# Kernel tuning notes

Hardware: AMD Instinct MI355X
Metric: run time of the kernel (lower is better)

## Reference

```python
import jax, jax.numpy as jnp
import numpy as np

N, E, D, DE, DH = 8000, 15000, 128, 16, 128
NUM_STEPS = 3


def setup_inputs() -> dict:
    key = jax.random.key(0)
    ks = jax.random.split(key, 10)
    s = lambda k, shape, scale: jax.random.normal(k, shape, jnp.float32) * scale
    return {
        "x": jax.random.normal(ks[0], (N, D), jnp.float32),
        "edge_attr": jax.random.normal(ks[1], (E, DE), jnp.float32),
        "W0": s(ks[2], (D, D), 0.08),   # lin0
        "b0": jnp.zeros((D,), jnp.float32),
        "W1": s(ks[3], (DE, DH), 0.2),  # edge net layer 1
        "b1": jnp.zeros((DH,), jnp.float32),
        "W2": s(ks[4], (DH, D * D), 0.02),  # edge net layer 2 -> D*D
        "b2": jnp.zeros((D * D,), jnp.float32),
        "root": s(ks[5], (D, D), 0.08),  # NNConv root weight
        "bias": jnp.zeros((D,), jnp.float32),  # NNConv bias
        "Wm": s(ks[6], (2 * D, D), 0.08),  # message_layer
        "bm": jnp.zeros((D,), jnp.float32),
        "edge_index": jax.random.randint(ks[7], (2, E), 0, N, jnp.int32),
    }


def reference(x, edge_attr, W0, b0, W1, b1, W2, b2, root, bias, Wm, bm, edge_index):
    n, d = x.shape
    src, dst = edge_index[0], edge_index[1]  # source_to_target flow (PyG default)
    # edge-conditioned weight matrices, identical across steps since edge_attr is fixed: [E, D, D]
    ew = (jax.nn.relu(edge_attr @ W1 + b1) @ W2 + b2).reshape(-1, d, d)
    init = x
    out = jax.nn.relu(x @ W0 + b0)
    for _ in range(NUM_STEPS):
        # gather source features, per-edge matvec, scatter-add to destinations
        msg = jnp.einsum('ed,edo->eo', out[src], ew)  # [E, D]
        agg = jax.ops.segment_sum(msg, dst, num_segments=n)  # [N, D]
        m = jax.nn.relu(agg + out @ root + bias)  # NNConv with root_weight + bias, then relu
        out = jnp.concatenate([m, out], axis=1) @ Wm + bm  # message_layer
    return out + init
```

## Files before the change

kernel.cpp:

```cpp
#include <hip/hip_runtime.h>

#define NE   15000
#define NVX  8000
#define EPAD 15104
#define NT_E 118

typedef __attribute__((ext_vector_type(8))) short short8;
typedef __attribute__((ext_vector_type(4))) float f32x4;

static __device__ __forceinline__ unsigned short f2b(float f){
  unsigned int u = __float_as_uint(f);
  u += 0x7fffu + ((u >> 16) & 1u);
  return (unsigned short)(u >> 16);
}

__global__ __launch_bounds__(256) void k_cvt(const float* __restrict__ in,
                                             unsigned short* __restrict__ out, int n){
  int i = (blockIdx.x * 256 + threadIdx.x) * 4;
  if (i >= n) return;
  float4 v = *(const float4*)(in + i);
  ushort4 o;
  o.x = f2b(v.x); o.y = f2b(v.y); o.z = f2b(v.z); o.w = f2b(v.w);
  *(ushort4*)(out + i) = o;
}

__global__ __launch_bounds__(256) void k_h1(const float* __restrict__ ea,
                                            const float* __restrict__ W1,
                                            const float* __restrict__ b1,
                                            float* __restrict__ h1T){
  __shared__ float sW1[16*128];
  __shared__ float sb1[128];
  int t = threadIdx.x;
  #pragma unroll
  for (int i = 0; i < 8; ++i) sW1[i*256 + t] = W1[i*256 + t];
  if (t < 128) sb1[t] = b1[t];
  __syncthreads();
  int e = blockIdx.x * 64 + (t & 63);
  int hg = t >> 6;
  bool valid = e < NE;
  int esafe = valid ? e : 0;
  float a[16];
  #pragma unroll
  for (int i = 0; i < 4; ++i){
    float4 v = *(const float4*)(ea + (size_t)esafe*16 + i*4);
    a[i*4+0]=v.x; a[i*4+1]=v.y; a[i*4+2]=v.z; a[i*4+3]=v.w;
  }
  for (int hh = 0; hh < 32; ++hh){
    int h = hg*32 + hh;
    float s = sb1[h];
    #pragma unroll
    for (int k = 0; k < 16; ++k) s = fmaf(a[k], sW1[k*128 + h], s);
    s = fmaxf(s, 0.f);
    h1T[(size_t)h*EPAD + e] = valid ? s : 0.f;
  }
}

__global__ __launch_bounds__(256) void k_wt(const float* __restrict__ W2,
                                            const float* __restrict__ b2,
                                            const float* __restrict__ W0,
                                            const float* __restrict__ root,
                                            const float* __restrict__ Wm,
                                            unsigned short* __restrict__ W2T,
                                            unsigned short* __restrict__ sWt){
  int b = blockIdx.x;
  const float* src;
  unsigned short* out;
  if (b < 128)      { src = W2 + (size_t)b*16384; out = W2T + (size_t)b*16384; }
  else if (b == 128){ src = b2;                   out = W2T + (size_t)128*16384; }
  else {
    int s = b - 129;
    out = sWt + (size_t)s*16384;
    src = (s==0) ? W0 : (s==1) ? root : (s==2) ? Wm : (Wm + 128*128);
  }
  int t = threadIdx.x;
  int o = t & 127, half = t >> 7;
  for (int it = 0; it < 8; ++it){
    int d0 = half*64 + it*8;
    unsigned int pk[4];
    #pragma unroll
    for (int j = 0; j < 4; ++j){
      float v0 = src[(size_t)(d0 + 2*j    )*128 + o];
      float v1 = src[(size_t)(d0 + 2*j + 1)*128 + o];
      pk[j] = (unsigned int)f2b(v0) | ((unsigned int)f2b(v1) << 16);
    }
    unsigned int off = (unsigned int)(o*256 + d0*2) ^ (((unsigned int)(o & 7)) << 4);
    *(uint4*)((char*)out + off) = make_uint4(pk[0], pk[1], pk[2], pk[3]);
  }
}

__global__ __launch_bounds__(512,2) void k_big(const unsigned short* __restrict__ outcur,
                                               const unsigned short* __restrict__ W2T,
                                               const float* __restrict__ h1T,
                                               const int* __restrict__ eidx,
                                               float* __restrict__ agg){
  __shared__ __align__(16) unsigned short sX[128*128];
  int t = threadIdx.x, l = t & 63, w = t >> 6;
  int tile = blockIdx.x >> 1, par = blockIdx.x & 1;
  int e0 = tile * 128;
  {
    int r = t >> 2, q = t & 3;
    int e = e0 + r;
    int srow = eidx[e < NE ? e : NE-1];
    const uint4* gp = (const uint4*)(outcur + (size_t)srow*128);
    #pragma unroll
    for (int i = 0; i < 4; ++i){
      uint4 v = gp[q*4 + i];
      unsigned off = (unsigned)((q*64 + i*16) ^ ((r & 7) << 4));
      *(uint4*)((char*)sX + r*256 + off) = v;
    }
  }
  __syncthreads();
  short8 af[8][4];
  #pragma unroll
  for (int mf = 0; mf < 8; ++mf){
    int row = mf*16 + (l & 15);
    #pragma unroll
    for (int kf = 0; kf < 4; ++kf){
      unsigned off = (unsigned)((kf*64 + ((l >> 4)*16)) ^ ((row & 7) << 4));
      af[mf][kf] = *(const short8*)((const char*)sX + row*256 + off);
    }
  }
  f32x4 acc[8];
  #pragma unroll
  for (int mf = 0; mf < 8; ++mf) acc[mf] = (f32x4){0.f,0.f,0.f,0.f};
  int colc = w*16 + (l & 15);
  unsigned offB[4];
  #pragma unroll
  for (int kf = 0; kf < 4; ++kf)
    offB[kf] = (unsigned)((colc*256 + kf*64 + ((l >> 4)*16)) ^ ((colc & 7) << 4));
  const float* hbase = h1T + e0 + ((l >> 4) << 2);
  const char* wb2 = (const char*)W2T;
  const f32x4 zf = (f32x4){0.f,0.f,0.f,0.f};
  int nh = 64 + ((par == 0) ? 1 : 0);
  for (int hh = 0; hh < nh; ++hh){
    int h = (hh < 64) ? (par + 2*hh) : 128;
    const char* wb = wb2 + (size_t)h * 32768;
    short8 bq[4];
    #pragma unroll
    for (int kf = 0; kf < 4; ++kf) bq[kf] = *(const short8*)(wb + offB[kf]);
    const float* hp = hbase + (size_t)h * EPAD;
    #pragma unroll
    for (int half = 0; half < 2; ++half){
      f32x4 Y[4];
      #pragma unroll
      for (int kf = 0; kf < 4; ++kf)
        #pragma unroll
        for (int m4 = 0; m4 < 4; ++m4)
          Y[m4] = __builtin_amdgcn_mfma_f32_16x16x32_bf16(af[half*4+m4][kf], bq[kf],
                    (kf == 0) ? zf : Y[m4], 0, 0, 0);
      f32x4 hv[4];
      if (hh < 64){
        #pragma unroll
        for (int m4 = 0; m4 < 4; ++m4) hv[m4] = *(const f32x4*)(hp + (half*4+m4)*16);
      } else {
        #pragma unroll
        for (int m4 = 0; m4 < 4; ++m4){
          int rb = e0 + (half*4+m4)*16 + ((l >> 4) << 2);
          #pragma unroll
          for (int j = 0; j < 4; ++j) hv[m4][j] = (rb + j < NE) ? 1.f : 0.f;
        }
      }
      #pragma unroll
      for (int m4 = 0; m4 < 4; ++m4)
        #pragma unroll
        for (int j = 0; j < 4; ++j)
          acc[half*4+m4][j] = fmaf(hv[m4][j], Y[m4][j], acc[half*4+m4][j]);
    }
  }
  #pragma unroll
  for (int mf = 0; mf < 8; ++mf){
    #pragma unroll
    for (int j = 0; j < 4; ++j){
      int e = e0 + mf*16 + ((l >> 4) << 2) + j;
      int dst = (e < NE) ? eidx[NE + e] : 0;
      atomicAdd(agg + (size_t)dst*128 + colc, acc[mf][j]);
    }
  }
}

__global__ __launch_bounds__(256,2) void k_gsm(const unsigned short* __restrict__ Aa,
                                               const unsigned short* __restrict__ Wa,
                                               const unsigned short* __restrict__ Ab,
                                               const unsigned short* __restrict__ Wb,
                                               const float* __restrict__ addin,
                                               float* __restrict__ clr,
                                               const float* __restrict__ bias,
                                               int do_relu,
                                               unsigned short* __restrict__ outb,
                                               float* __restrict__ outf){
  __shared__ __align__(16) unsigned short sA[64*128];
  __shared__ __align__(16) unsigned short sW[128*128];
  int t = threadIdx.x, l = t & 63, w = t >> 6;
  int r0 = blockIdx.x * 64;
  f32x4 acc[4][2];
  #pragma unroll
  for (int mf = 0; mf < 4; ++mf)
    #pragma unroll
    for (int nf = 0; nf < 2; ++nf)
      acc[mf][nf] = (f32x4){0.f,0.f,0.f,0.f};
  const unsigned short* A = Aa;
  const unsigned short* W = Wa;
  for (int pass = 0; pass < 2; ++pass){
    if (pass == 1){
      if (Ab == nullptr) break;
      A = Ab; W = Wb;
      __syncthreads();
    }
    {
      const uint4* gp = (const uint4*)((const char*)A + (size_t)r0*256);
      uint4* lp = (uint4*)sA;
      #pragma unroll
      for (int i = 0; i < 4; ++i) lp[i*256 + t] = gp[i*256 + t];
      const uint4* gw = (const uint4*)W;
      uint4* lw = (uint4*)sW;
      #pragma unroll
      for (int i = 0; i < 8; ++i) lw[i*256 + t] = gw[i*256 + t];
    }
    __syncthreads();
    short8 af[4][4];
    #pragma unroll
    for (int mf = 0; mf < 4; ++mf)
      #pragma unroll
      for (int kf = 0; kf < 4; ++kf)
        af[mf][kf] = *(const short8*)((const char*)sA + (mf*16 + (l & 15))*256 + kf*64 + ((l >> 4)*16));
    #pragma unroll
    for (int nf = 0; nf < 2; ++nf){
      int col = w*32 + nf*16 + (l & 15);
      unsigned int swz = ((unsigned int)(col & 7)) << 4;
      #pragma unroll
      for (int kf = 0; kf < 4; ++kf){
        short8 bfr = *(const short8*)((const char*)sW +
                        (((unsigned int)(col*256 + kf*64 + ((l >> 4)*16))) ^ swz));
        #pragma unroll
        for (int mf = 0; mf < 4; ++mf)
          acc[mf][nf] = __builtin_amdgcn_mfma_f32_16x16x32_bf16(af[mf][kf], bfr, acc[mf][nf], 0, 0, 0);
      }
    }
  }
  #pragma unroll
  for (int mf = 0; mf < 4; ++mf){
    #pragma unroll
    for (int nf = 0; nf < 2; ++nf){
      #pragma unroll
      for (int j = 0; j < 4; ++j){
        int r = r0 + mf*16 + ((l >> 4) << 2) + j;
        int c = w*32 + nf*16 + (l & 15);
        float v = acc[mf][nf][j];
        if (addin) v += addin[(size_t)r*128 + c];
        if (clr)   clr[(size_t)r*128 + c] = 0.f;
        v += bias[c];
        if (do_relu) v = fmaxf(v, 0.f);
        if (outb) outb[(size_t)r*128 + c] = f2b(v);
        if (outf) outf[(size_t)r*128 + c] = v;
      }
    }
  }
}

extern "C" void kernel_launch(void* const* d_in, const int* in_sizes, int n_in,
                              void* d_out, int out_size, void* d_ws, size_t ws_size,
                              hipStream_t stream){
  (void)in_sizes; (void)n_in; (void)out_size; (void)ws_size;
  const float* x    = (const float*)d_in[0];
  const float* ea   = (const float*)d_in[1];
  const float* W0   = (const float*)d_in[2];
  const float* b0   = (const float*)d_in[3];
  const float* W1   = (const float*)d_in[4];
  const float* b1   = (const float*)d_in[5];
  const float* W2   = (const float*)d_in[6];
  const float* b2   = (const float*)d_in[7];
  const float* root = (const float*)d_in[8];
  const float* bias = (const float*)d_in[9];
  const float* Wm   = (const float*)d_in[10];
  const float* bm   = (const float*)d_in[11];
  const int*   eidx = (const int*)d_in[12];

  char* p = (char*)d_ws;
  unsigned short* W2T = (unsigned short*)p; p += (size_t)129*32768;
  unsigned short* sWt = (unsigned short*)p; p += (size_t)4*32768;
  float*          h1T = (float*)p;          p += (size_t)128*EPAD*4;
  unsigned short* xb  = (unsigned short*)p; p += (size_t)NVX*128*2;
  unsigned short* oA  = (unsigned short*)p; p += (size_t)NVX*128*2;
  unsigned short* oB  = (unsigned short*)p; p += (size_t)NVX*128*2;
  unsigned short* mB  = (unsigned short*)p; p += (size_t)NVX*128*2;
  float*          agg = (float*)p;          p += (size_t)NVX*128*4;

  k_cvt<<<1000, 256, 0, stream>>>(x, xb, NVX*128);
  k_h1 <<<EPAD/64, 256, 0, stream>>>(ea, W1, b1, h1T);
  k_wt <<<133,  256, 0, stream>>>(W2, b2, W0, root, Wm, W2T, sWt);
  k_gsm<<<125, 256, 0, stream>>>(xb, sWt + 0*16384,
                                 (const unsigned short*)nullptr, (const unsigned short*)nullptr,
                                 (const float*)nullptr, (float*)nullptr, b0, 1, oA, (float*)nullptr);
  unsigned short* cur = oA;
  unsigned short* nxt = oB;
  for (int s = 0; s < 3; ++s){
    if (s == 0) hipMemsetAsync(agg, 0, (size_t)NVX*128*4, stream);
    k_big<<<2*NT_E, 512, 0, stream>>>(cur, W2T, h1T, eidx, agg);
    k_gsm<<<125, 256, 0, stream>>>(cur, sWt + 1*16384,
                                   (const unsigned short*)nullptr, (const unsigned short*)nullptr,
                                   agg, (s < 2) ? agg : (float*)nullptr, bias, 1, mB, (float*)nullptr);
    if (s < 2){
      k_gsm<<<125, 256, 0, stream>>>(mB, sWt + 2*16384, cur, sWt + 3*16384,
                                     (const float*)nullptr, (float*)nullptr, bm, 0, nxt, (float*)nullptr);
    } else {
      k_gsm<<<125, 256, 0, stream>>>(mB, sWt + 2*16384, cur, sWt + 3*16384,
                                     x, (float*)nullptr, bm, 0, (unsigned short*)nullptr, (float*)d_out);
    }
    unsigned short* tsw = cur; cur = nxt; nxt = tsw;
  }
}
```

Baseline: 424.2 us.

## Prefetch W2 fragments one step ahead and stage h1 tile in LDS

The edge-net kernel now software-pipelines the per-h W2 B-fragment loads, fetching the next hidden unit's fragments while the current MFMAs run. The block's slice of h1T (64 rows x 128 edges) is staged into shared memory once up front instead of being read from global memory inside the loop. The bias (h=128) step is peeled out of the loop for the even-parity blocks. Shared memory grows by 32 KB and launch bounds drop to one 512-thread block per CU minimum, so occupancy may fall while register pressure rises from the double-buffered fragments.

```diff
diff --git a/kernel.cpp b/kernel.cpp
--- a/kernel.cpp
+++ b/kernel.cpp
@@ -88,15 +88,26 @@
   }
 }
 
-__global__ __launch_bounds__(512,2) void k_big(const unsigned short* __restrict__ outcur,
+__global__ __launch_bounds__(512,1) void k_big(const unsigned short* __restrict__ outcur,
                                                const unsigned short* __restrict__ W2T,
                                                const float* __restrict__ h1T,
                                                const int* __restrict__ eidx,
                                                float* __restrict__ agg){
   __shared__ __align__(16) unsigned short sX[128*128];
+  __shared__ __align__(16) float          sH[64*128];
   int t = threadIdx.x, l = t & 63, w = t >> 6;
   int tile = blockIdx.x >> 1, par = blockIdx.x & 1;
   int e0 = tile * 128;
+  int colc = w*16 + (l & 15);
+  unsigned offB[4];
+  #pragma unroll
+  for (int kf = 0; kf < 4; ++kf)
+    offB[kf] = (unsigned)((colc*256 + kf*64 + ((l >> 4)*16)) ^ ((colc & 7) << 4));
+  const char* wb2 = (const char*)W2T;
+  short8 bq[4];
+  #pragma unroll
+  for (int kf = 0; kf < 4; ++kf)
+    bq[kf] = *(const short8*)(wb2 + (size_t)par*32768 + offB[kf]);
   {
     int r = t >> 2, q = t & 3;
     int e = e0 + r;
@@ -109,6 +120,14 @@
       *(uint4*)((char*)sX + r*256 + off) = v;
     }
   }
+  {
+    #pragma unroll
+    for (int i = 0; i < 4; ++i){
+      int n = i*512 + t;
+      int row = n >> 5, c4 = n & 31;
+      ((f32x4*)sH)[n] = ((const f32x4*)(h1T + (size_t)(par + 2*row)*EPAD + e0))[c4];
+    }
+  }
   __syncthreads();
   short8 af[8][4];
   #pragma unroll
@@ -123,22 +142,15 @@
   f32x4 acc[8];
   #pragma unroll
   for (int mf = 0; mf < 8; ++mf) acc[mf] = (f32x4){0.f,0.f,0.f,0.f};
-  int colc = w*16 + (l & 15);
-  unsigned offB[4];
-  #pragma unroll
-  for (int kf = 0; kf < 4; ++kf)
-    offB[kf] = (unsigned)((colc*256 + kf*64 + ((l >> 4)*16)) ^ ((colc & 7) << 4));
-  const float* hbase = h1T + e0 + ((l >> 4) << 2);
-  const char* wb2 = (const char*)W2T;
   const f32x4 zf = (f32x4){0.f,0.f,0.f,0.f};
-  int nh = 64 + ((par == 0) ? 1 : 0);
-  for (int hh = 0; hh < nh; ++hh){
-    int h = (hh < 64) ? (par + 2*hh) : 128;
-    const char* wb = wb2 + (size_t)h * 32768;
-    short8 bq[4];
-    #pragma unroll
-    for (int kf = 0; kf < 4; ++kf) bq[kf] = *(const short8*)(wb + offB[kf]);
-    const float* hp = hbase + (size_t)h * EPAD;
+  #pragma unroll 2
+  for (int hh = 0; hh < 64; ++hh){
+    int hn = par + 2*hh + 2;
+    if (hn > 128) hn = 128;
+    short8 bqn[4];
+    #pragma unroll
+    for (int kf = 0; kf < 4; ++kf)
+      bqn[kf] = *(const short8*)(wb2 + (size_t)hn*32768 + offB[kf]);
     #pragma unroll
     for (int half = 0; half < 2; ++half){
       f32x4 Y[4];
@@ -149,22 +161,35 @@
           Y[m4] = __builtin_amdgcn_mfma_f32_16x16x32_bf16(af[half*4+m4][kf], bq[kf],
                     (kf == 0) ? zf : Y[m4], 0, 0, 0);
       f32x4 hv[4];
-      if (hh < 64){
-        #pragma unroll
-        for (int m4 = 0; m4 < 4; ++m4) hv[m4] = *(const f32x4*)(hp + (half*4+m4)*16);
-      } else {
-        #pragma unroll
-        for (int m4 = 0; m4 < 4; ++m4){
-          int rb = e0 + (half*4+m4)*16 + ((l >> 4) << 2);
-          #pragma unroll
-          for (int j = 0; j < 4; ++j) hv[m4][j] = (rb + j < NE) ? 1.f : 0.f;
-        }
-      }
+      #pragma unroll
+      for (int m4 = 0; m4 < 4; ++m4)
+        hv[m4] = *(const f32x4*)((const char*)sH + hh*512 + (half*4+m4)*64 + ((l >> 4)*16));
       #pragma unroll
       for (int m4 = 0; m4 < 4; ++m4)
         #pragma unroll
         for (int j = 0; j < 4; ++j)
           acc[half*4+m4][j] = fmaf(hv[m4][j], Y[m4][j], acc[half*4+m4][j]);
+    }
+    #pragma unroll
+    for (int kf = 0; kf < 4; ++kf) bq[kf] = bqn[kf];
+  }
+  if (par == 0){
+    #pragma unroll
+    for (int half = 0; half < 2; ++half){
+      f32x4 Y[4];
+      #pragma unroll
+      for (int kf = 0; kf < 4; ++kf)
+        #pragma unroll
+        for (int m4 = 0; m4 < 4; ++m4)
+          Y[m4] = __builtin_amdgcn_mfma_f32_16x16x32_bf16(af[half*4+m4][kf], bq[kf],
+                    (kf == 0) ? zf : Y[m4], 0, 0, 0);
+      #pragma unroll
+      for (int m4 = 0; m4 < 4; ++m4){
+        int rb = e0 + (half*4+m4)*16 + ((l >> 4) << 2);
+        #pragma unroll
+        for (int j = 0; j < 4; ++j)
+          if (rb + j < NE) acc[half*4+m4][j] += Y[m4][j];
+      }
     }
   }
   #pragma unroll
```

Result: faster. 359.9 us (-15.1%).

## Restructure edge-conditioned matvec kernel with smaller tiles and fragment-linear W2 layout

Applied to the files above, without the earlier changes.

The main edge kernel now uses 64-edge tiles split across output halves and h-parity, giving 940 blocks of 256 threads instead of 236 blocks of 512. W2T is stored in an MFMA-fragment-linear layout so each wave reads its weight fragments contiguously, and the next h slice is double-buffered in registers. The MFMA operands are swapped so edges sit on the N dimension. h1 values and destination indices are staged in shared memory, and s_setprio raises wave priority around the MFMA blocks. The aim is more occupancy, better latency hiding and less scattered global traffic, at the cost of more blocks re-gathering source rows and reloading W2.

```diff
diff --git a/kernel.cpp b/kernel.cpp
--- a/kernel.cpp
+++ b/kernel.cpp
@@ -3,7 +3,7 @@
 #define NE   15000
 #define NVX  8000
 #define EPAD 15104
-#define NT_E 118
+#define NT_E 235
 
 typedef __attribute__((ext_vector_type(8))) short short8;
 typedef __attribute__((ext_vector_type(4))) float f32x4;
@@ -65,6 +65,7 @@
   int b = blockIdx.x;
   const float* src;
   unsigned short* out;
+  bool fraglin = (b < 129);
   if (b < 128)      { src = W2 + (size_t)b*16384; out = W2T + (size_t)b*16384; }
   else if (b == 128){ src = b2;                   out = W2T + (size_t)128*16384; }
   else {
@@ -83,20 +84,35 @@
       float v1 = src[(size_t)(d0 + 2*j + 1)*128 + o];
       pk[j] = (unsigned int)f2b(v0) | ((unsigned int)f2b(v1) << 16);
     }
-    unsigned int off = (unsigned int)(o*256 + d0*2) ^ (((unsigned int)(o & 7)) << 4);
+    unsigned int off;
+    if (fraglin)
+      off = (unsigned)((o >> 4)*4096 + (d0 >> 5)*1024 + (((d0 >> 3) & 3)*16 + (o & 15))*16);
+    else
+      off = ((unsigned)(o*256 + d0*2)) ^ (((unsigned)(o & 7)) << 4);
     *(uint4*)((char*)out + off) = make_uint4(pk[0], pk[1], pk[2], pk[3]);
   }
 }
 
-__global__ __launch_bounds__(512,2) void k_big(const unsigned short* __restrict__ outcur,
+__global__ __launch_bounds__(256,3) void k_big(const unsigned short* __restrict__ outcur,
                                                const unsigned short* __restrict__ W2T,
                                                const float* __restrict__ h1T,
                                                const int* __restrict__ eidx,
                                                float* __restrict__ agg){
-  __shared__ __align__(16) unsigned short sX[128*128];
+  __shared__ __align__(16) unsigned short sX[64*128];
+  __shared__ __align__(16) float          sH[64*64];
+  __shared__ int sD[64];
   int t = threadIdx.x, l = t & 63, w = t >> 6;
-  int tile = blockIdx.x >> 1, par = blockIdx.x & 1;
-  int e0 = tile * 128;
+  unsigned bid = blockIdx.x;
+  int tile = bid >> 2, oh = (bid >> 1) & 1, par = bid & 1;
+  int e0 = tile * 64;
+  const char* wb2 = (const char*)W2T;
+  unsigned offA = (unsigned)((oh*4 + w)*4096 + l*16);
+  short8 aqA[4], aqB[4];
+  {
+    const char* wb = wb2 + (size_t)par*32768 + offA;
+    #pragma unroll
+    for (int kf = 0; kf < 4; ++kf) aqA[kf] = *(const short8*)(wb + kf*1024);
+  }
   {
     int r = t >> 2, q = t & 3;
     int e = e0 + r;
@@ -109,72 +125,91 @@
       *(uint4*)((char*)sX + r*256 + off) = v;
     }
   }
+  {
+    #pragma unroll
+    for (int i = 0; i < 4; ++i){
+      int n = i*256 + t;
+      int row = n >> 4, c = n & 15;
+      ((f32x4*)sH)[n] = ((const f32x4*)(h1T + (size_t)(par + 2*row)*EPAD + e0))[c];
+    }
+  }
+  if (t < 64){
+    int e = e0 + t;
+    sD[t] = (e < NE) ? eidx[NE + e] : 0;
+  }
   __syncthreads();
-  short8 af[8][4];
-  #pragma unroll
-  for (int mf = 0; mf < 8; ++mf){
-    int row = mf*16 + (l & 15);
+  short8 bfr[4][4];
+  #pragma unroll
+  for (int nf = 0; nf < 4; ++nf){
+    int row = nf*16 + (l & 15);
     #pragma unroll
     for (int kf = 0; kf < 4; ++kf){
       unsigned off = (unsigned)((kf*64 + ((l >> 4)*16)) ^ ((row & 7) << 4));
-      af[mf][kf] = *(const short8*)((const char*)sX + row*256 + off);
-    }
-  }
-  f32x4 acc[8];
-  #pragma unroll
-  for (int mf = 0; mf < 8; ++mf) acc[mf] = (f32x4){0.f,0.f,0.f,0.f};
-  int colc = w*16 + (l & 15);
-  unsigned offB[4];
-  #pragma unroll
-  for (int kf = 0; kf < 4; ++kf)
-    offB[kf] = (unsigned)((colc*256 + kf*64 + ((l >> 4)*16)) ^ ((colc & 7) << 4));
-  const float* hbase = h1T + e0 + ((l >> 4) << 2);
-  const char* wb2 = (const char*)W2T;
+      bfr[nf][kf] = *(const short8*)((const char*)sX + row*256 + off);
+    }
+  }
+  f32x4 acc[4];
+  #pragma unroll
+  for (int nf = 0; nf < 4; ++nf) acc[nf] = (f32x4){0.f,0.f,0.f,0.f};
   const f32x4 zf = (f32x4){0.f,0.f,0.f,0.f};
-  int nh = 64 + ((par == 0) ? 1 : 0);
-  for (int hh = 0; hh < nh; ++hh){
-    int h = (hh < 64) ? (par + 2*hh) : 128;
-    const char* wb = wb2 + (size_t)h * 32768;
-    short8 bq[4];
-    #pragma unroll
-    for (int kf = 0; kf < 4; ++kf) bq[kf] = *(const short8*)(wb + offB[kf]);
-    const float* hp = hbase + (size_t)h * EPAD;
-    #pragma unroll
-    for (int half = 0; half < 2; ++half){
-      f32x4 Y[4];
-      #pragma unroll
-      for (int kf = 0; kf < 4; ++kf)
+  int ecol = l & 15;
+  for (int hh = 0; hh < 64; hh += 2){
+    {
+      const char* wb = wb2 + (size_t)(par + 2*(hh+1))*32768 + offA;
+      #pragma unroll
+      for (int kf = 0; kf < 4; ++kf) aqB[kf] = *(const short8*)(wb + kf*1024);
+    }
+    __builtin_amdgcn_s_setprio(1);
+    #pragma unroll
+    for (int nf = 0; nf < 4; ++nf){
+      f32x4 Y = __builtin_amdgcn_mfma_f32_16x16x32_bf16(aqA[0], bfr[nf][0], zf, 0, 0, 0);
+      Y = __builtin_amdgcn_mfma_f32_16x16x32_bf16(aqA[1], bfr[nf][1], Y, 0, 0, 0);
+      Y = __builtin_amdgcn_mfma_f32_16x16x32_bf16(aqA[2], bfr[nf][2], Y, 0, 0, 0);
+      Y = __builtin_amdgcn_mfma_f32_16x16x32_bf16(aqA[3], bfr[nf][3], Y, 0, 0, 0);
+      float hs = sH[hh*64 + nf*16 + ecol];
+      #pragma unroll
+      for (int j = 0; j < 4; ++j) acc[nf][j] = fmaf(hs, Y[j], acc[nf][j]);
+    }
+    __builtin_amdgcn_s_setprio(0);
+    {
+      int kb = par + 2*(hh+2);
+      if (kb > 128) kb = 128;
+      const char* wb = wb2 + (size_t)kb*32768 + offA;
+      #pragma unroll
+      for (int kf = 0; kf < 4; ++kf) aqA[kf] = *(const short8*)(wb + kf*1024);
+    }
+    __builtin_amdgcn_s_setprio(1);
+    #pragma unroll
+    for (int nf = 0; nf < 4; ++nf){
+      f32x4 Y = __builtin_amdgcn_mfma_f32_16x16x32_bf16(aqB[0], bfr[nf][0], zf, 0, 0, 0);
+      Y = __builtin_amdgcn_mfma_f32_16x16x32_bf16(aqB[1], bfr[nf][1], Y, 0, 0, 0);
+      Y = __builtin_amdgcn_mfma_f32_16x16x32_bf16(aqB[2], bfr[nf][2], Y, 0, 0, 0);
+      Y = __builtin_amdgcn_mfma_f32_16x16x32_bf16(aqB[3], bfr[nf][3], Y, 0, 0, 0);
+      float hs = sH[(hh+1)*64 + nf*16 + ecol];
+      #pragma unroll
+      for (int j = 0; j < 4; ++j) acc[nf][j] = fmaf(hs, Y[j], acc[nf][j]);
+    }
+    __builtin_amdgcn_s_setprio(0);
+  }
+  if (par == 0){
+    #pragma unroll
+    for (int nf = 0; nf < 4; ++nf){
+      f32x4 Y = __builtin_amdgcn_mfma_f32_16x16x32_bf16(aqA[0], bfr[nf][0], zf, 0, 0, 0);
+      Y = __builtin_amdgcn_mfma_f32_16x16x32_bf16(aqA[1], bfr[nf][1], Y, 0, 0, 0);
+      Y = __builtin_amdgcn_mfma_f32_16x16x32_bf16(aqA[2], bfr[nf][2], Y, 0, 0, 0);
+      Y = __builtin_amdgcn_mfma_f32_16x16x32_bf16(aqA[3], bfr[nf][3], Y, 0, 0, 0);
+      if (e0 + nf*16 + ecol < NE){
         #pragma unroll
-        for (int m4 = 0; m4 < 4; ++m4)
-          Y[m4] = __builtin_amdgcn_mfma_f32_16x16x32_bf16(af[half*4+m4][kf], bq[kf],
-                    (kf == 0) ? zf : Y[m4], 0, 0, 0);
-      f32x4 hv[4];
-      if (hh < 64){
-        #pragma unroll
-        for (int m4 = 0; m4 < 4; ++m4) hv[m4] = *(const f32x4*)(hp + (half*4+m4)*16);
-      } else {
-        #pragma unroll
-        for (int m4 = 0; m4 < 4; ++m4){
-          int rb = e0 + (half*4+m4)*16 + ((l >> 4) << 2);
-          #pragma unroll
-          for (int j = 0; j < 4; ++j) hv[m4][j] = (rb + j < NE) ? 1.f : 0.f;
-        }
+        for (int j = 0; j < 4; ++j) acc[nf][j] += Y[j];
       }
-      #pragma unroll
-      for (int m4 = 0; m4 < 4; ++m4)
-        #pragma unroll
-        for (int j = 0; j < 4; ++j)
-          acc[half*4+m4][j] = fmaf(hv[m4][j], Y[m4][j], acc[half*4+m4][j]);
-    }
-  }
-  #pragma unroll
-  for (int mf = 0; mf < 8; ++mf){
-    #pragma unroll
-    for (int j = 0; j < 4; ++j){
-      int e = e0 + mf*16 + ((l >> 4) << 2) + j;
-      int dst = (e < NE) ? eidx[NE + e] : 0;
-      atomicAdd(agg + (size_t)dst*128 + colc, acc[mf][j]);
-    }
+    }
+  }
+  #pragma unroll
+  for (int nf = 0; nf < 4; ++nf){
+    int dst = sD[nf*16 + ecol];
+    float* ap = agg + (size_t)dst*128 + oh*64 + w*16 + ((l >> 4) << 2);
+    #pragma unroll
+    for (int j = 0; j < 4; ++j) atomicAdd(ap + j, acc[nf][j]);
   }
 }
 
@@ -295,7 +330,7 @@
   unsigned short* nxt = oB;
   for (int s = 0; s < 3; ++s){
     if (s == 0) hipMemsetAsync(agg, 0, (size_t)NVX*128*4, stream);
-    k_big<<<2*NT_E, 512, 0, stream>>>(cur, W2T, h1T, eidx, agg);
+    k_big<<<NT_E*4, 256, 0, stream>>>(cur, W2T, h1T, eidx, agg);
     k_gsm<<<125, 256, 0, stream>>>(cur, sWt + 1*16384,
                                    (const unsigned short*)nullptr, (const unsigned short*)nullptr,
                                    agg, (s < 2) ? agg : (float*)nullptr, bias, 1, mB, (float*)nullptr);
```

Result: slower. 456.1 us (+7.5%).

## Double-buffer W2 tiles in LDS via async loads and stage h1 in LDS

Applied to the files above, without the earlier changes.

The edge-weight GEMM kernel now streams each 32KB W2T slice into a pair of LDS buffers with global_load_lds. The load for the next h step is issued while MFMAs run on the current one. The h1 coefficients for the block's 64 h values are preloaded into LDS with nontemporal loads, and MFMA chains are interleaved with the scaling FMAs under raised wave priority. This is meant to hide global-load latency on W2 and h1 inside the inner loop. In exchange, LDS use grows to 96KB and launch bounds drop to one block per CU, which lowers occupancy.

```diff
diff --git a/kernel.cpp b/kernel.cpp
--- a/kernel.cpp
+++ b/kernel.cpp
@@ -88,15 +88,39 @@
   }
 }
 
-__global__ __launch_bounds__(512,2) void k_big(const unsigned short* __restrict__ outcur,
+__global__ __launch_bounds__(512,1) void k_big(const unsigned short* __restrict__ outcur,
                                                const unsigned short* __restrict__ W2T,
                                                const float* __restrict__ h1T,
                                                const int* __restrict__ eidx,
                                                float* __restrict__ agg){
-  __shared__ __align__(16) unsigned short sX[128*128];
+  __shared__ __align__(16) char lds[3*32768];
+  char* wbufA = lds;
+  char* wbufB = lds + 32768;
+  float* sH   = (float*)(lds + 65536);
   int t = threadIdx.x, l = t & 63, w = t >> 6;
   int tile = blockIdx.x >> 1, par = blockIdx.x & 1;
   int e0 = tile * 128;
+  int colc = w*16 + (l & 15);
+  unsigned lq16 = (unsigned)((l >> 4) * 16);
+  unsigned swzc = ((unsigned)(colc & 7)) << 4;
+  unsigned bofs0 = (unsigned)(colc*256 +   0 + lq16) ^ swzc;
+  unsigned bofs1 = (unsigned)(colc*256 +  64 + lq16) ^ swzc;
+  unsigned bofs2 = (unsigned)(colc*256 + 128 + lq16) ^ swzc;
+  unsigned bofs3 = (unsigned)(colc*256 + 192 + lq16) ^ swzc;
+  const char* gsrc = (const char*)W2T + w*4096 + l*16;
+
+#define KB_STAGE(LB, H) {                                                      \
+    const char* g_ = gsrc + (size_t)(H)*32768;                                 \
+    char* l_ = (LB) + w*4096;           \
+    _Pragma("unroll")                                                          \
+    for (int r_ = 0; r_ < 4; ++r_)                                             \
+      __builtin_amdgcn_global_load_lds(                                        \
+        (const __attribute__((address_space(1))) unsigned int*)(g_ + r_*1024), \
+        (__attribute__((address_space(3))) unsigned int*)(l_ + r_*1024),       \
+        16, 0, 0);                                                             \
+  }
+
+  KB_STAGE(wbufA, par);
   {
     int r = t >> 2, q = t & 3;
     int e = e0 + r;
@@ -106,7 +130,16 @@
     for (int i = 0; i < 4; ++i){
       uint4 v = gp[q*4 + i];
       unsigned off = (unsigned)((q*64 + i*16) ^ ((r & 7) << 4));
-      *(uint4*)((char*)sX + r*256 + off) = v;
+      *(uint4*)(wbufB + r*256 + off) = v;
+    }
+  }
+  {
+    #pragma unroll
+    for (int i = 0; i < 4; ++i){
+      int n = i*512 + t;
+      int row = n >> 5, c4 = n & 31;
+      const f32x4* src = ((const f32x4*)(h1T + (size_t)(par + 2*row)*EPAD + e0)) + c4;
+      ((f32x4*)sH)[n] = __builtin_nontemporal_load(src);
     }
   }
   __syncthreads();
@@ -117,56 +150,80 @@
     #pragma unroll
     for (int kf = 0; kf < 4; ++kf){
       unsigned off = (unsigned)((kf*64 + ((l >> 4)*16)) ^ ((row & 7) << 4));
-      af[mf][kf] = *(const short8*)((const char*)sX + row*256 + off);
-    }
-  }
+      af[mf][kf] = *(const short8*)(wbufB + row*256 + off);
+    }
+  }
+  __syncthreads();
   f32x4 acc[8];
   #pragma unroll
   for (int mf = 0; mf < 8; ++mf) acc[mf] = (f32x4){0.f,0.f,0.f,0.f};
-  int colc = w*16 + (l & 15);
-  unsigned offB[4];
-  #pragma unroll
-  for (int kf = 0; kf < 4; ++kf)
-    offB[kf] = (unsigned)((colc*256 + kf*64 + ((l >> 4)*16)) ^ ((colc & 7) << 4));
-  const float* hbase = h1T + e0 + ((l >> 4) << 2);
-  const char* wb2 = (const char*)W2T;
   const f32x4 zf = (f32x4){0.f,0.f,0.f,0.f};
-  int nh = 64 + ((par == 0) ? 1 : 0);
-  for (int hh = 0; hh < nh; ++hh){
-    int h = (hh < 64) ? (par + 2*hh) : 128;
-    const char* wb = wb2 + (size_t)h * 32768;
-    short8 bq[4];
-    #pragma unroll
-    for (int kf = 0; kf < 4; ++kf) bq[kf] = *(const short8*)(wb + offB[kf]);
-    const float* hp = hbase + (size_t)h * EPAD;
-    #pragma unroll
-    for (int half = 0; half < 2; ++half){
-      f32x4 Y[4];
-      #pragma unroll
-      for (int kf = 0; kf < 4; ++kf)
-        #pragma unroll
-        for (int m4 = 0; m4 < 4; ++m4)
-          Y[m4] = __builtin_amdgcn_mfma_f32_16x16x32_bf16(af[half*4+m4][kf], bq[kf],
-                    (kf == 0) ? zf : Y[m4], 0, 0, 0);
-      f32x4 hv[4];
-      if (hh < 64){
-        #pragma unroll
-        for (int m4 = 0; m4 < 4; ++m4) hv[m4] = *(const f32x4*)(hp + (half*4+m4)*16);
-      } else {
-        #pragma unroll
-        for (int m4 = 0; m4 < 4; ++m4){
-          int rb = e0 + (half*4+m4)*16 + ((l >> 4) << 2);
-          #pragma unroll
-          for (int j = 0; j < 4; ++j) hv[m4][j] = (rb + j < NE) ? 1.f : 0.f;
-        }
-      }
-      #pragma unroll
-      for (int m4 = 0; m4 < 4; ++m4)
-        #pragma unroll
-        for (int j = 0; j < 4; ++j)
-          acc[half*4+m4][j] = fmaf(hv[m4][j], Y[m4][j], acc[half*4+m4][j]);
-    }
-  }
+
+#define KB_CHAIN(DST, MF)                                                            \
+    DST = __builtin_amdgcn_mfma_f32_16x16x32_bf16(af[MF][0], bq0, zf,  0,0,0);       \
+    DST = __builtin_amdgcn_mfma_f32_16x16x32_bf16(af[MF][1], bq1, DST, 0,0,0);       \
+    DST = __builtin_amdgcn_mfma_f32_16x16x32_bf16(af[MF][2], bq2, DST, 0,0,0);       \
+    DST = __builtin_amdgcn_mfma_f32_16x16x32_bf16(af[MF][3], bq3, DST, 0,0,0);
+
+#define KB_FMA(MF, Y)                                                                \
+    _Pragma("unroll")                                                                \
+    for (int j_ = 0; j_ < 4; ++j_)                                                   \
+      acc[MF][j_] = fmaf(hvv[MF][j_], Y[j_], acc[MF][j_]);
+
+#define KB_ITER(CURB, NXTB, HH) {                                                    \
+    asm volatile("s_waitcnt vmcnt(0)" ::: "memory");      \
+    __builtin_amdgcn_sched_barrier(0);                                               \
+    short8 bq0 = *(const short8*)((CURB) + bofs0);                                   \
+    short8 bq1 = *(const short8*)((CURB) + bofs1);                                   \
+    short8 bq2 = *(const short8*)((CURB) + bofs2);                                   \
+    short8 bq3 = *(const short8*)((CURB) + bofs3);                                   \
+    f32x4 hvv[8];                                                                    \
+    _Pragma("unroll")                                                                \
+    for (int mf_ = 0; mf_ < 8; ++mf_)                                                \
+      hvv[mf_] = *(const f32x4*)((const char*)sH + (HH)*512 + mf_*64 + lq16);        \
+    __builtin_amdgcn_sched_barrier(0);          \
+    int hn_ = par + 2*((HH) + 1); if (hn_ > 128) hn_ = 128;                          \
+    KB_STAGE(NXTB, hn_);                                                             \
+    __builtin_amdgcn_sched_barrier(0);           \
+    f32x4 Yc, Yp;                                                                    \
+    __builtin_amdgcn_s_setprio(1);                                                   \
+    KB_CHAIN(Yc, 0)                                                                  \
+    Yp = Yc; KB_CHAIN(Yc, 1) KB_FMA(0, Yp)                                           \
+    Yp = Yc; KB_CHAIN(Yc, 2) KB_FMA(1, Yp)                                           \
+    Yp = Yc; KB_CHAIN(Yc, 3) KB_FMA(2, Yp)                                           \
+    Yp = Yc; KB_CHAIN(Yc, 4) KB_FMA(3, Yp)                                           \
+    Yp = Yc; KB_CHAIN(Yc, 5) KB_FMA(4, Yp)                                           \
+    Yp = Yc; KB_CHAIN(Yc, 6) KB_FMA(5, Yp)                                           \
+    Yp = Yc; KB_CHAIN(Yc, 7) KB_FMA(6, Yp)                                           \
+    __builtin_amdgcn_s_setprio(0);                                                   \
+    KB_FMA(7, Yc)                                                                    \
+  }
+
+  for (int hh = 0; hh < 64; hh += 2){
+    KB_ITER(wbufA, wbufB, hh)
+    KB_ITER(wbufB, wbufA, hh+1)
+  }
+  if (par == 0){
+    asm volatile("s_waitcnt vmcnt(0)" ::: "memory");
+    __builtin_amdgcn_sched_barrier(0);
+    short8 bq0 = *(const short8*)(wbufA + bofs0);
+    short8 bq1 = *(const short8*)(wbufA + bofs1);
+    short8 bq2 = *(const short8*)(wbufA + bofs2);
+    short8 bq3 = *(const short8*)(wbufA + bofs3);
+    #pragma unroll
+    for (int mf = 0; mf < 8; ++mf){
+      f32x4 Y;
+      KB_CHAIN(Y, mf)
+      int rb = e0 + mf*16 + ((l >> 4) << 2);
+      #pragma unroll
+      for (int j = 0; j < 4; ++j)
+        if (rb + j < NE) acc[mf][j] += Y[j];
+    }
+  }
+#undef KB_ITER
+#undef KB_FMA
+#undef KB_CHAIN
+#undef KB_STAGE
   #pragma unroll
   for (int mf = 0; mf < 8; ++mf){
     #pragma unroll
```

Result: slower. 875.3 us (+106.3%).
